# Kernel tuning notes

Hardware: AMD Instinct MI355X
Metric: run time of the kernel (lower is better)

## Reference

```python
import jax, jax.numpy as jnp
import numpy as np

INPUT, HIDDEN = 40, 250
B, T = 256, 512


def lstm_layer(x_seq, W_ih, W_hh, b_ih, b_hh):
    """x_seq: [B,T,D_in] -> [B,T,H]. PyTorch gate order: i,f,g,o."""
    # Precompute input contribution with one big GEMM: [B,T,4H]
    xg = jnp.einsum('btd,gd->btg', x_seq, W_ih) + b_ih + b_hh
    xg_t = jnp.transpose(xg, (1, 0, 2))  # [T,B,4H]
    H = W_hh.shape[1]
    h0 = jnp.zeros((x_seq.shape[0], H), dtype=x_seq.dtype)
    c0 = jnp.zeros_like(h0)

    def step(carry, g_in):
        h, c = carry
        g = g_in + h @ W_hh.T  # [B,4H]
        i = jax.nn.sigmoid(g[:, :H])
        f = jax.nn.sigmoid(g[:, H:2 * H])
        gg = jnp.tanh(g[:, 2 * H:3 * H])
        o = jax.nn.sigmoid(g[:, 3 * H:])
        c = f * c + i * gg
        h = o * jnp.tanh(c)
        return (h, c), h

    _, hs = jax.lax.scan(step, (h0, c0), xg_t)  # hs: [T,B,H]
    return jnp.transpose(hs, (1, 0, 2))


def setup_inputs() -> dict:
    key = jax.random.key(0)
    ks = jax.random.split(key, 12)
    s_in = 1.0 / np.sqrt(HIDDEN)  # PyTorch LSTM init scale
    u = lambda k, shape: jax.random.uniform(k, shape, jnp.float32, -s_in, s_in)
    return {
        'x': jax.random.normal(ks[0], (B, T, INPUT), jnp.float32),
        'W_ih0': u(ks[1], (4 * HIDDEN, INPUT)),
        'W_hh0': u(ks[2], (4 * HIDDEN, HIDDEN)),
        'b_ih0': u(ks[3], (4 * HIDDEN,)),
        'b_hh0': u(ks[4], (4 * HIDDEN,)),
        'W_ih1': u(ks[5], (4 * HIDDEN, HIDDEN)),
        'W_hh1': u(ks[6], (4 * HIDDEN, HIDDEN)),
        'b_ih1': u(ks[7], (4 * HIDDEN,)),
        'b_hh1': u(ks[8], (4 * HIDDEN,)),
        'W_lin': u(ks[9], (1, HIDDEN)),
        'b_lin': u(ks[10], (1,)),
    }


def reference(x, W_ih0, W_hh0, b_ih0, b_hh0, W_ih1, W_hh1, b_ih1, b_hh1, W_lin, b_lin):
    h1 = lstm_layer(x, W_ih0, W_hh0, b_ih0, b_hh0)   # [B,T,H]
    h2 = lstm_layer(h1, W_ih1, W_hh1, b_ih1, b_hh1)  # [B,T,H]
    y = jnp.einsum('bth,oh->bto', h2, W_lin) + b_lin  # [B,T,1]
    return jax.nn.sigmoid(y)
```

## Files before the change

### kernel.cpp

```cpp
#include <hip/hip_runtime.h>
#include <cstdint>

#define B_TOT 256
#define T_LEN 512
#define NX    40
#define NH    250
#define HP    256
#define XP    64
#define K0    (XP + HP)
#define K1    (HP + HP)
#define MB    32
#define NU    16
#define NR    64
#define RING  8
#define LDSK  520
#define NFLAG 4096
#define GSTRIDE 256
#define RSTEP (B_TOT * HP / 2)
#define XCD_AT(w) ((w) * 4 + 1)
#define BAR_IDX 3
#define GETREG_XCC 63508

typedef __attribute__((ext_vector_type(8))) short short8;
typedef __attribute__((ext_vector_type(4))) float float4v;

__device__ __forceinline__ unsigned short f2bf(float f) {
  unsigned u = __float_as_uint(f);
  u += 0x7FFFu + ((u >> 16) & 1u);
  return (unsigned short)(u >> 16);
}
__device__ __forceinline__ float bf2f(unsigned short h) {
  return __uint_as_float(((unsigned)h) << 16);
}
__device__ __forceinline__ float sigm(float x) { return 1.0f / (1.0f + __expf(-x)); }
__device__ __forceinline__ float tanh_f(float x) {
  float e = __expf(-2.0f * fabsf(x));
  float t = (1.0f - e) / (1.0f + e);
  return copysignf(t, x);
}
__device__ __forceinline__ int ld_flag(const int* p) {
  return __hip_atomic_load(p, __ATOMIC_RELAXED, __HIP_MEMORY_SCOPE_AGENT);
}
__device__ __forceinline__ unsigned ld_lic(const unsigned* p) {
  return __hip_atomic_load(p, __ATOMIC_RELAXED, __HIP_MEMORY_SCOPE_AGENT);
}
__device__ __forceinline__ void inv_l1() {
  asm volatile("buffer_inv\n\ts_waitcnt vmcnt(0)" ::: "memory");
  __builtin_amdgcn_sched_barrier(0);
}
__device__ __forceinline__ void drain_vm() {
  asm volatile("s_waitcnt vmcnt(0)" ::: "memory");
  __builtin_amdgcn_sched_barrier(0);
}
template <bool FAST>
__device__ __forceinline__ unsigned ldh(const unsigned* p) {
  if (FAST) return *p;
  return ld_lic(p);
}
template <bool FAST>
__device__ __forceinline__ void sth(unsigned* p, unsigned v) {
  if (FAST) *p = v;
  else __hip_atomic_store(p, v, __ATOMIC_RELAXED, __HIP_MEMORY_SCOPE_AGENT);
}

template <int KSTEPS, int LAYER, bool FAST>
__device__ __forceinline__ void run_layer(
    int tid, int gg, int b0, int u0,
    const float* __restrict__ x, float* __restrict__ out, float blinv,
    unsigned short* __restrict__ h1bc, unsigned short* __restrict__ h2bc,
    int* __restrict__ c0s, int* __restrict__ c1s,
    unsigned short (*WL)[LDSK], unsigned short (*inA2)[LDSK],
    float* biasS, float* wlinS) {
  const int lane = tid & 63, wv = tid >> 6;
  const int quad = lane >> 4, l15 = lane & 15;
  const int Mt = wv & 1, Np = wv >> 1;
  const int gb = b0 >> 5;
  const int irow = tid >> 3, icol = tid & 7;

  const int* ownS = (LAYER ? c1s : c0s) + lane * 4;
  const int* othS = (LAYER ? c0s : c1s) + lane * 4;
  int* mysub = (LAYER ? c1s : c0s) + (wv * 16 + gg) * 4;

  short8 wfrag[2][KSTEPS];
#pragma unroll
  for (int ks = 0; ks < KSTEPS; ++ks) {
#pragma unroll
    for (int i = 0; i < 2; ++i)
      wfrag[i][ks] = *(const short8*)&WL[Np * 32 + i * 16 + l15][ks * 32 + quad * 8];
  }

  float4v b4A = *(const float4v*)&biasS[Np * 32 + quad * 4];
  float4v b4B = *(const float4v*)&biasS[Np * 32 + 16 + quad * 4];

  float xr[10];
  if (LAYER == 0 && tid < 128) {
    int b = tid >> 2, c = tid & 3;
    const float* xp0 = x + ((size_t)(b0 + b) * T_LEN + 0) * NX + c * 10;
#pragma unroll
    for (int j = 0; j < 10; ++j) xr[j] = xp0[j];
  }

  float cA = 0.f, cB = 0.f;

#pragma unroll 1
  for (int t = 0; t < T_LEN; ++t) {
    {
      const int thrOwn = t;
      const int thrOth = LAYER ? (t + 1) : (t - RING + 1);
      while (ld_flag(ownS) < thrOwn) __builtin_amdgcn_s_sleep(1);
      while (ld_flag(othS) < thrOth) __builtin_amdgcn_s_sleep(1);
    }
    if (!FAST) __syncthreads();
    if (FAST && (LAYER == 1 || t > 0)) inv_l1();

    unsigned short (*inbuf)[LDSK] = inA2 + (t & 1) * MB;

    if (LAYER == 0) {
      unsigned v[16];
      if (t > 0) {
        const unsigned* s1 = (const unsigned*)h1bc +
            ((size_t)((t - 1) & (RING - 1)) * RSTEP + (size_t)gb * 4096);
#pragma unroll
        for (int k = 0; k < 16; ++k) v[k] = ldh<FAST>(s1 + tid + k * 256);
      }
      if (tid < 128) {
        int b = tid >> 2, c = tid & 3;
#pragma unroll
        for (int j = 0; j < 10; ++j) inbuf[b][c * 10 + j] = f2bf(xr[j]);
        if (t + 1 < T_LEN) {
          const float* xp = x + ((size_t)(b0 + b) * T_LEN + (size_t)(t + 1)) * NX + c * 10;
#pragma unroll
          for (int j = 0; j < 10; ++j) xr[j] = xp[j];
        }
      }
      if (t > 0) {
#pragma unroll
        for (int k = 0; k < 16; ++k)
          ((unsigned*)&inbuf[irow][0])[32 + k * 8 + icol] = v[k];
      }
    } else {
      const unsigned* s1 = (const unsigned*)h1bc +
          ((size_t)(t & (RING - 1)) * RSTEP + (size_t)gb * 4096);
      unsigned va[16], vb[16];
#pragma unroll
      for (int k = 0; k < 16; ++k) va[k] = ldh<FAST>(s1 + tid + k * 256);
      if (t > 0) {
        const unsigned* s2 = (const unsigned*)h2bc +
            ((size_t)((t - 1) & (RING - 1)) * RSTEP + (size_t)gb * 4096);
#pragma unroll
        for (int k = 0; k < 16; ++k) vb[k] = ldh<FAST>(s2 + tid + k * 256);
      }
#pragma unroll
      for (int k = 0; k < 16; ++k) {
        unsigned* row = (unsigned*)&inbuf[irow][0];
        row[k * 8 + icol] = va[k];
        if (t > 0) row[128 + k * 8 + icol] = vb[k];
      }
    }
    __syncthreads();

    float4v acc0 = {0.f, 0.f, 0.f, 0.f};
    float4v acc1 = {0.f, 0.f, 0.f, 0.f};
#pragma unroll
    for (int ks = 0; ks < KSTEPS; ++ks) {
      short8 a = *(const short8*)&inbuf[Mt * 16 + l15][ks * 32 + quad * 8];
      acc0 = __builtin_amdgcn_mfma_f32_16x16x32_bf16(wfrag[0][ks], a, acc0, 0, 0, 0);
      acc1 = __builtin_amdgcn_mfma_f32_16x16x32_bf16(wfrag[1][ks], a, acc1, 0, 0, 0);
    }

    float hA, hB;
    {
      float i0 = sigm(acc0[0] + b4A[0]);
      float f0 = sigm(acc0[1] + b4A[1]);
      float g0 = tanh_f(acc0[2] + b4A[2]);
      float o0 = sigm(acc0[3] + b4A[3]);
      cA = f0 * cA + i0 * g0;
      hA = o0 * tanh_f(cA);
      float i1 = sigm(acc1[0] + b4B[0]);
      float f1 = sigm(acc1[1] + b4B[1]);
      float g1 = tanh_f(acc1[2] + b4B[2]);
      float o1 = sigm(acc1[3] + b4B[3]);
      cB = f1 * cB + i1 * g1;
      hB = o1 * tanh_f(cB);
    }
    {
      float hA2 = __shfl_xor(hA, 16);
      float hB2 = __shfl_xor(hB, 16);
      if ((quad & 1) == 0) {
        unsigned dwA = (unsigned)f2bf(hA) | ((unsigned)f2bf(hA2) << 16);
        unsigned dwB = (unsigned)f2bf(hB) | ((unsigned)f2bf(hB2) << 16);
        unsigned* dst = (unsigned*)(LAYER ? h2bc : h1bc);
        size_t base = (size_t)(t & (RING - 1)) * RSTEP + (size_t)gb * 4096 +
                      (size_t)gg * 256 + (size_t)(Mt * 16 + l15) * 8;
        sth<FAST>(dst + base + Np * 4 + (quad >> 1), dwA);
        sth<FAST>(dst + base + Np * 4 + 2 + (quad >> 1), dwB);
      }
    }

    if (FAST) {
      drain_vm();
      if (lane == 0) sth<true>((unsigned*)mysub, (unsigned)(t + 1));
    } else {
      __syncthreads();
      if (lane == 0) sth<false>((unsigned*)mysub, (unsigned)(t + 1));
    }

    if (LAYER == 1 && t > 0 && tid < 16) {
      int eb2 = 2 * gg + (tid >> 3), uc = tid & 7;
      float sum = 0.f;
#pragma unroll
      for (int j = 0; j < 4; ++j) {
        short8 hvv = *(const short8*)&inbuf[eb2][HP + uc * 32 + j * 8];
#pragma unroll
        for (int e = 0; e < 8; ++e)
          sum += bf2f((unsigned short)hvv[e]) * wlinS[uc * 32 + j * 8 + e];
      }
      sum += __shfl_xor(sum, 1);
      sum += __shfl_xor(sum, 2);
      sum += __shfl_xor(sum, 4);
      if ((tid & 7) == 0)
        out[(size_t)(b0 + eb2) * T_LEN + (t - 1)] = sigm(sum + blinv);
    }
  }

  if (LAYER == 1) {
    if (wv == 0) {
      const int* sl = c1s + lane * 4;
      while (ld_flag(sl) < T_LEN) __builtin_amdgcn_s_sleep(1);
    }
    __syncthreads();
    if (FAST) inv_l1();
    if (tid < 16) {
      int eb2 = 2 * gg + (tid >> 3), uc = tid & 7;
      const unsigned* base = (const unsigned*)h2bc +
          ((size_t)(511 & (RING - 1)) * RSTEP + (size_t)gb * 4096);
      float sum = 0.f;
#pragma unroll
      for (int g = 0; g < 2; ++g) {
        const unsigned* src = base + (size_t)(2 * uc + g) * 256 + eb2 * 8;
#pragma unroll
        for (int j = 0; j < 8; ++j) {
          unsigned dw = ldh<FAST>(src + j);
          sum += bf2f((unsigned short)(dw & 0xFFFFu)) * wlinS[uc * 32 + g * 16 + 2 * j];
          sum += bf2f((unsigned short)(dw >> 16)) * wlinS[uc * 32 + g * 16 + 2 * j + 1];
        }
      }
      sum += __shfl_xor(sum, 1);
      sum += __shfl_xor(sum, 2);
      sum += __shfl_xor(sum, 4);
      if ((tid & 7) == 0)
        out[(size_t)(b0 + eb2) * T_LEN + 511] = sigm(sum + blinv);
    }
  }
}

extern "C" __global__ void __launch_bounds__(256, 1) lstm_persist(
    const float* __restrict__ x,
    const float* __restrict__ Wih0, const float* __restrict__ Whh0,
    const float* __restrict__ bih0, const float* __restrict__ bhh0,
    const float* __restrict__ Wih1, const float* __restrict__ Whh1,
    const float* __restrict__ bih1, const float* __restrict__ bhh1,
    const float* __restrict__ Wlin, const float* __restrict__ blin,
    float* __restrict__ out,
    unsigned short* __restrict__ h1bc, unsigned short* __restrict__ h2bc,
    int* __restrict__ cnt) {
  __shared__ unsigned short WL[NR][LDSK];
  __shared__ unsigned short inA[2 * MB][LDSK];
  __shared__ float biasS[NR];
  __shared__ float wlinS[HP];

  const int tid = threadIdx.x;
  const int wg = blockIdx.x;

  const unsigned xcc = ((unsigned)__builtin_amdgcn_s_getreg(GETREG_XCC)) & 15u;
  if (tid == 0) {
    __hip_atomic_store(cnt + XCD_AT(wg), (int)xcc, __ATOMIC_RELAXED,
                       __HIP_MEMORY_SCOPE_AGENT);
    __hip_atomic_fetch_add(cnt + BAR_IDX, 1, __ATOMIC_ACQ_REL,
                           __HIP_MEMORY_SCOPE_AGENT);
    while (__hip_atomic_load(cnt + BAR_IDX, __ATOMIC_ACQUIRE,
                             __HIP_MEMORY_SCOPE_AGENT) < 256)
      __builtin_amdgcn_s_sleep(8);
  }
  __syncthreads();
  int* sx = (int*)&inA[0][0];
  sx[tid] = __hip_atomic_load(cnt + XCD_AT(tid), __ATOMIC_RELAXED,
                              __HIP_MEMORY_SCOPE_AGENT);
  __syncthreads();
  const int myv = sx[wg];
  int rank = 0;
  unsigned long long hist = 0;
  bool ok = true;
  for (int j = 0; j < 256; ++j) {
    int v = sx[j];
    if ((unsigned)v > 7u) { ok = false; v = 0; }
    hist += 1ull << (v * 8);
    if (v == myv && j < wg) rank++;
  }
  ok = ok && (hist == 0x2020202020202020ull);
  __syncthreads();

  int layer, gb, gg;
  if (ok) { gb = myv;       layer = rank >> 4;    gg = rank & 15; }
  else    { layer = wg >> 7; gb = (wg >> 4) & 7;  gg = wg & 15;   }
  const int b0 = gb * MB, u0 = gg * NU;

  {
    const float* Wih = layer ? Wih1 : Wih0;
    const float* Whh = layer ? Whh1 : Whh0;
    const float* bi = layer ? bih1 : bih0;
    const float* bh = layer ? bhh1 : bhh0;
    const int K = layer ? K1 : K0;
    const int xw = layer ? NH : NX;
    const int xofs = layer ? HP : XP;
    int r = tid >> 2, c = tid & 3;
    int lu = r >> 2, g = r & 3, ug = u0 + lu;
    int row = g * NH + ug;
    int kq = K >> 2;
    for (int k = c * kq; k < (c + 1) * kq; ++k) {
      float v = 0.f;
      if (ug < NH) {
        if (k < xw) v = Wih[(size_t)row * xw + k];
        else if (k >= xofs && k < xofs + NH) v = Whh[(size_t)row * NH + (k - xofs)];
      }
      WL[r][k] = f2bf(v);
    }
    if (tid < NR) {
      int lu2 = tid >> 2, g2 = tid & 3, ug2 = u0 + lu2;
      biasS[tid] = (ug2 < NH) ? (bi[g2 * NH + ug2] + bh[g2 * NH + ug2]) : 0.f;
    }
    if (tid < HP) wlinS[tid] = (tid < NH) ? Wlin[tid] : 0.f;
    for (int i = tid; i < 2 * MB * LDSK; i += 256) ((unsigned short*)inA)[i] = 0;
  }
  __syncthreads();

  float blinv = blin[0];
  int* c0s = cnt + gb * GSTRIDE;
  int* c1s = cnt + (8 + gb) * GSTRIDE;

  if (ok) {
    if (layer == 0)
      run_layer<K0 / 32, 0, true>(tid, gg, b0, u0, x, out, blinv, h1bc, h2bc,
                                  c0s, c1s, WL, inA, biasS, wlinS);
    else
      run_layer<K1 / 32, 1, true>(tid, gg, b0, u0, x, out, blinv, h1bc, h2bc,
                                  c0s, c1s, WL, inA, biasS, wlinS);
  } else {
    if (layer == 0)
      run_layer<K0 / 32, 0, false>(tid, gg, b0, u0, x, out, blinv, h1bc, h2bc,
                                   c0s, c1s, WL, inA, biasS, wlinS);
    else
      run_layer<K1 / 32, 1, false>(tid, gg, b0, u0, x, out, blinv, h1bc, h2bc,
                                   c0s, c1s, WL, inA, biasS, wlinS);
  }
}

extern "C" __global__ void prep_zero(int* cnt) {
  int i = blockIdx.x * 256 + threadIdx.x;
  if (i < NFLAG)
    __hip_atomic_store(cnt + i, 0, __ATOMIC_RELAXED, __HIP_MEMORY_SCOPE_AGENT);
}

extern "C" void kernel_launch(void* const* d_in, const int* in_sizes, int n_in,
                              void* d_out, int out_size, void* d_ws, size_t ws_size,
                              hipStream_t stream) {
  const float* x    = (const float*)d_in[0];
  const float* Wih0 = (const float*)d_in[1];
  const float* Whh0 = (const float*)d_in[2];
  const float* bih0 = (const float*)d_in[3];
  const float* bhh0 = (const float*)d_in[4];
  const float* Wih1 = (const float*)d_in[5];
  const float* Whh1 = (const float*)d_in[6];
  const float* bih1 = (const float*)d_in[7];
  const float* bhh1 = (const float*)d_in[8];
  const float* Wlin = (const float*)d_in[9];
  const float* blin = (const float*)d_in[10];
  float* out = (float*)d_out;

  unsigned short* h1bc = (unsigned short*)d_ws;
  unsigned short* h2bc = h1bc + (size_t)RING * B_TOT * HP;
  int* cnt = (int*)((char*)d_ws + 2u * (size_t)RING * B_TOT * HP * sizeof(unsigned short));

  hipLaunchKernelGGL(prep_zero, dim3(16), dim3(256), 0, stream, cnt);

  void* args[] = {&x, &Wih0, &Whh0, &bih0, &bhh0, &Wih1, &Whh1, &bih1, &bhh1,
                  &Wlin, &blin, &out, &h1bc, &h2bc, &cnt};
  hipLaunchCooperativeKernel((void*)lstm_persist, dim3(256), dim3(256), args, 0u, stream);
}
```

Measured before the change: 1.313 ms.

## Restructure inter-block flag polling to a single-wave min-of-four wait

```diff
diff --git a/kernel.cpp b/kernel.cpp
--- a/kernel.cpp
+++ b/kernel.cpp
@@ -17,8 +17,8 @@
 #define NFLAG 4096
 #define GSTRIDE 256
 #define RSTEP (B_TOT * HP / 2)
-#define XCD_AT(w) ((w) * 4 + 1)
-#define BAR_IDX 3
+#define XCD_AT(w) (((w) >> 4) * GSTRIDE + 64 + ((w) & 15))
+#define BAR_IDX 80
 #define GETREG_XCC 63508
 
 typedef __attribute__((ext_vector_type(8))) short short8;
@@ -40,6 +40,11 @@
 }
 __device__ __forceinline__ int ld_flag(const int* p) {
   return __hip_atomic_load(p, __ATOMIC_RELAXED, __HIP_MEMORY_SCOPE_AGENT);
+}
+__device__ __forceinline__ int min4_flag(const int* p) {
+  int a = ld_flag(p + 0), b = ld_flag(p + 1);
+  int c = ld_flag(p + 2), d = ld_flag(p + 3);
+  return min(min(a, b), min(c, d));
 }
 __device__ __forceinline__ unsigned ld_lic(const unsigned* p) {
   return __hip_atomic_load(p, __ATOMIC_RELAXED, __HIP_MEMORY_SCOPE_AGENT);
@@ -77,9 +82,7 @@
   const int gb = b0 >> 5;
   const int irow = tid >> 3, icol = tid & 7;
 
-  const int* ownS = (LAYER ? c1s : c0s) + lane * 4;
-  const int* othS = (LAYER ? c0s : c1s) + lane * 4;
-  int* mysub = (LAYER ? c1s : c0s) + (wv * 16 + gg) * 4;
+  int* mysub = (LAYER ? c1s : c0s) + gg * 4 + wv;
 
   short8 wfrag[2][KSTEPS];
 #pragma unroll
@@ -104,39 +107,35 @@
 
 #pragma unroll 1
   for (int t = 0; t < T_LEN; ++t) {
-    {
-      const int thrOwn = t;
-      const int thrOth = LAYER ? (t + 1) : (t - RING + 1);
-      while (ld_flag(ownS) < thrOwn) __builtin_amdgcn_s_sleep(1);
-      while (ld_flag(othS) < thrOth) __builtin_amdgcn_s_sleep(1);
-    }
-    if (!FAST) __syncthreads();
+    if (wv == 0 && lane < 32) {
+      const int* sl = ((lane < 16) ? c0s : c1s) + (lane & 15) * 4;
+      int thr;
+      if (LAYER == 0) thr = (lane < 16) ? t : (t - RING + 1);
+      else            thr = (lane < 16) ? (t + 1) : t;
+      while (min4_flag(sl) < thr) {
+        __builtin_amdgcn_s_sleep(1);
+      }
+    }
+    __syncthreads();
     if (FAST && (LAYER == 1 || t > 0)) inv_l1();
 
     unsigned short (*inbuf)[LDSK] = inA2 + (t & 1) * MB;
 
     if (LAYER == 0) {
-      unsigned v[16];
       if (t > 0) {
         const unsigned* s1 = (const unsigned*)h1bc +
             ((size_t)((t - 1) & (RING - 1)) * RSTEP + (size_t)gb * 4096);
+        unsigned v[16];
 #pragma unroll
         for (int k = 0; k < 16; ++k) v[k] = ldh<FAST>(s1 + tid + k * 256);
+#pragma unroll
+        for (int k = 0; k < 16; ++k)
+          ((unsigned*)&inbuf[irow][0])[32 + k * 8 + icol] = v[k];
       }
       if (tid < 128) {
         int b = tid >> 2, c = tid & 3;
 #pragma unroll
         for (int j = 0; j < 10; ++j) inbuf[b][c * 10 + j] = f2bf(xr[j]);
-        if (t + 1 < T_LEN) {
-          const float* xp = x + ((size_t)(b0 + b) * T_LEN + (size_t)(t + 1)) * NX + c * 10;
-#pragma unroll
-          for (int j = 0; j < 10; ++j) xr[j] = xp[j];
-        }
-      }
-      if (t > 0) {
-#pragma unroll
-        for (int k = 0; k < 16; ++k)
-          ((unsigned*)&inbuf[irow][0])[32 + k * 8 + icol] = v[k];
       }
     } else {
       const unsigned* s1 = (const unsigned*)h1bc +
@@ -158,6 +157,13 @@
       }
     }
     __syncthreads();
+
+    if (LAYER == 0 && tid < 128 && t + 1 < T_LEN) {
+      int b = tid >> 2, c = tid & 3;
+      const float* xp = x + ((size_t)(b0 + b) * T_LEN + (size_t)(t + 1)) * NX + c * 10;
+#pragma unroll
+      for (int j = 0; j < 10; ++j) xr[j] = xp[j];
+    }
 
     float4v acc0 = {0.f, 0.f, 0.f, 0.f};
     float4v acc1 = {0.f, 0.f, 0.f, 0.f};
@@ -224,9 +230,9 @@
   }
 
   if (LAYER == 1) {
-    if (wv == 0) {
+    if (wv == 0 && lane < 16) {
       const int* sl = c1s + lane * 4;
-      while (ld_flag(sl) < T_LEN) __builtin_amdgcn_s_sleep(1);
+      while (min4_flag(sl) < T_LEN) __builtin_amdgcn_s_sleep(1);
     }
     __syncthreads();
     if (FAST) inv_l1();
```

After: 1.332 ms. No clear change (+1.4%).
